# Kernel optimization log

Hardware: AMD Instinct MI355X
Metric: run time of the kernel (lower is better)

The kernel has to match this reference:

```python
import jax, jax.numpy as jnp
import numpy as np

F = 128          # num_features
NRBF = 20        # num_rbf_features
N_NODES = 25000
N_EDGES = 400000


def setup_inputs() -> dict:
    key = jax.random.key(0)
    ks = jax.random.split(key, 12)
    inp = {
        "idx_i": jax.random.randint(ks[0], (N_EDGES,), 0, N_NODES, dtype=jnp.int32),
        "idx_j": jax.random.randint(ks[1], (N_EDGES,), 0, N_NODES, dtype=jnp.int32),
        "rel_dir": jax.random.normal(ks[2], (N_EDGES, 3), dtype=jnp.float32),
        "rel_dist_cut": jax.random.uniform(ks[3], (N_EDGES,), dtype=jnp.float32),
        "rbf_features": jax.random.normal(ks[4], (N_EDGES, NRBF), dtype=jnp.float32),
        "scalar_features": jax.random.normal(ks[5], (N_NODES, F), dtype=jnp.float32),
        "vector_features": jax.random.normal(ks[6], (N_NODES, F, 3), dtype=jnp.float32),
        # scalar_network: Linear(F,F) -> SiLU -> Linear(F,3F)
        "W1": jax.random.normal(ks[7], (F, F), dtype=jnp.float32) / np.sqrt(F),
        "b1": jnp.zeros((F,), dtype=jnp.float32),
        "W2": jax.random.normal(ks[8], (3 * F, F), dtype=jnp.float32) / np.sqrt(F),
        "b2": jnp.zeros((3 * F,), dtype=jnp.float32),
        # rbf_network: Linear(NRBF, 3F)
        "Wr": jax.random.normal(ks[9], (3 * F, NRBF), dtype=jnp.float32) / np.sqrt(NRBF),
        "br": jnp.zeros((3 * F,), dtype=jnp.float32),
    }
    return inp


def reference(idx_i, idx_j, rel_dir, rel_dist_cut, rbf_features,
              scalar_features, vector_features, W1, b1, W2, b2, Wr, br):
    n_nodes = scalar_features.shape[0]
    # phi: per-node MLP -> [N, 3F]
    h = jax.nn.silu(scalar_features @ W1.T + b1)
    phi = h @ W2.T + b2
    # W: RBF-derived edge weights gated by cosine-cut distance -> [E, 3F]
    W = (rbf_features @ Wr.T + br) * rel_dist_cut[:, None]
    phi_W = phi[idx_j] * W                                  # [E, 3F]
    phi_W_vv, phi_W_ss, phi_W_vs = jnp.split(phi_W, 3, axis=-1)
    # scatter-add scalar residuals
    scalar_res = jax.ops.segment_sum(phi_W_ss, idx_i, num_segments=n_nodes)
    # per-edge vector messages [E, F, 3]
    vec_per_edge = (vector_features[idx_j] * phi_W_vv[..., None]
                    + phi_W_vs[..., None] * rel_dir[:, None, :])
    vector_res = jax.ops.segment_sum(vec_per_edge, idx_i, num_segments=n_nodes)
    return scalar_features + scalar_res, vector_features + vector_res
```

## Files before the change

### kernel.cpp

```cpp
#include <hip/hip_runtime.h>
#include <hip/hip_fp16.h>

#define F 128
#define F3 384
#define NRBF 20
#define NPB 16
#define CHUNK 64
#define PSN 32

typedef unsigned int u32;
typedef _Float16 half8 __attribute__((ext_vector_type(8)));
typedef float floatx4 __attribute__((ext_vector_type(4)));

__device__ __forceinline__ float2 uph(u32 u) {
    __half2 h = *(__half2*)&u;
    return __half22float2(h);
}
__device__ __forceinline__ u32 pkh(float a, float b) {
    __half2 h = __floats2half2_rn(a, b);
    return *(u32*)&h;
}

__device__ __forceinline__ float fdot2f(u32 a, u32 b, float c) {
#if defined(__has_builtin)
#if __has_builtin(__builtin_amdgcn_fdot2)
    typedef _Float16 h2 __attribute__((ext_vector_type(2)));
    return __builtin_amdgcn_fdot2(*(h2*)&a, *(h2*)&b, c, false);
#else
    float2 fa = uph(a), fb = uph(b);
    return fmaf(fa.x, fb.x, fmaf(fa.y, fb.y, c));
#endif
#else
    float2 fa = uph(a), fb = uph(b);
    return fmaf(fa.x, fb.x, fmaf(fa.y, fb.y, c));
#endif
}

__global__ void prep2_kernel(const float* __restrict__ Wr,
                             const float* __restrict__ W1, const float* __restrict__ W2,
                             u32* __restrict__ WrTh, _Float16* __restrict__ Wh,
                             const int* __restrict__ idx_i, int* __restrict__ counts,
                             int n_edges, int PKB) {
    int blk = blockIdx.x, tid = threadIdx.x;
    if (blk >= PKB) {
        int e = (blk - PKB) * 256 + tid;
        if (e < n_edges) atomicAdd(&counts[idx_i[e]], 1);
        return;
    }
    int t = blk * 256 + tid;
    if (t < 10 * F3) {
        int rr = t / F3, f = t % F3;
        WrTh[rr * F3 + f] = pkh(Wr[f * NRBF + 2 * rr], Wr[f * NRBF + 2 * rr + 1]);
        return;
    }
    int u = t - 10 * F3;
    if (u < (F + F3) * F) {
        int n = u >> 7, k = u & (F - 1);
        float w = (n < F) ? W1[n * F + k] : W2[(size_t)(n - F) * F + k];
        Wh[u] = (_Float16)w;
    }
}

#define SCAN_T 1024
#define SCAN_MAXN 25600
__launch_bounds__(SCAN_T)
__global__ void scan_lds_kernel(const int* __restrict__ counts, int* __restrict__ row_start,
                                int* __restrict__ cursor, int n) {
    __shared__ int sbuf[SCAN_MAXN];
    __shared__ int partial[SCAN_T];
    int t = threadIdx.x;
    for (int i = t; i < n; i += SCAN_T) sbuf[i] = counts[i];
    __syncthreads();
    int C = (n + SCAN_T - 1) / SCAN_T;
    int beg = t * C, end = min(beg + C, n);
    int sum = 0;
    for (int i = beg; i < end; i++) sum += sbuf[i];
    partial[t] = sum;
    __syncthreads();
    for (int off = 1; off < SCAN_T; off <<= 1) {
        int v = (t >= off) ? partial[t - off] : 0;
        __syncthreads();
        partial[t] += v;
        __syncthreads();
    }
    int base = (t == 0) ? 0 : partial[t - 1];
    for (int i = beg; i < end; i++) { int c = sbuf[i]; sbuf[i] = base; base += c; }
    __syncthreads();
    for (int i = t; i < n; i += SCAN_T) { int v = sbuf[i]; row_start[i] = v; cursor[i] = v; }
    if (t == SCAN_T - 1) row_start[n] = partial[SCAN_T - 1];
}

__launch_bounds__(1024)
__global__ void scan_kernel(const int* __restrict__ counts, int* __restrict__ row_start,
                            int* __restrict__ cursor, int n) {
    __shared__ int partial[1024];
    int t = threadIdx.x;
    int C = (n + 1023) / 1024;
    int beg = t * C, end = min(beg + C, n);
    int sum = 0;
    for (int i = beg; i < end; i++) sum += counts[i];
    partial[t] = sum;
    __syncthreads();
    for (int off = 1; off < 1024; off <<= 1) {
        int v = (t >= off) ? partial[t - off] : 0;
        __syncthreads();
        partial[t] += v;
        __syncthreads();
    }
    int base = (t == 0) ? 0 : partial[t - 1];
    for (int i = beg; i < end; i++) {
        int c = counts[i];
        row_start[i] = base; cursor[i] = base; base += c;
    }
    if (t == 1023) row_start[n] = partial[1023];
}

__global__ void scatter_kernel(const int* __restrict__ idx_i, int* __restrict__ cursor,
                               int* __restrict__ edge_order, int n_edges) {
    int e = blockIdx.x * blockDim.x + threadIdx.x;
    if (e < n_edges) {
        int p = atomicAdd(&cursor[idx_i[e]], 1);
        edge_order[p] = e;
    }
}

__launch_bounds__(128)
__global__ void phi_stage_kernel(const float* __restrict__ sf,
                                 const _Float16* __restrict__ Wh,
                                 const float* __restrict__ b1, const float* __restrict__ b2,
                                 const float* __restrict__ vf, __half* __restrict__ gbufh,
                                 int n_nodes) {
    __shared__ __align__(16) _Float16 stage[PSN * 768];
    _Float16 (*hl)[16][136] = reinterpret_cast<_Float16 (*)[16][136]>(stage);

    int tid = threadIdx.x;
    int lane = tid & 63;
    int wv = tid >> 6;
    int col = lane & 15;
    int kg = lane >> 4;
    int base = blockIdx.x * PSN;
    int row0 = base + wv * 16;

    half8 a1[4];
#pragma unroll
    for (int kb = 0; kb < 4; kb++) {
        int rr = row0 + col;
        if (rr >= n_nodes) rr = n_nodes - 1;
        const float4* xp = (const float4*)(sf + (size_t)rr * F + kb * 32 + kg * 8);
        float4 x0 = xp[0], x1 = xp[1];
        half8 a;
        a[0] = (_Float16)x0.x; a[1] = (_Float16)x0.y; a[2] = (_Float16)x0.z; a[3] = (_Float16)x0.w;
        a[4] = (_Float16)x1.x; a[5] = (_Float16)x1.y; a[6] = (_Float16)x1.z; a[7] = (_Float16)x1.w;
        a1[kb] = a;
    }

    floatx4 acc[8];
#pragma unroll
    for (int nt = 0; nt < 8; nt++) acc[nt] = (floatx4){0.f, 0.f, 0.f, 0.f};
#pragma unroll
    for (int nt = 0; nt < 8; nt++) {
#pragma unroll
        for (int kb = 0; kb < 4; kb++) {
            half8 b = *(const half8*)(Wh + (size_t)(nt * 16 + col) * F + kb * 32 + kg * 8);
            acc[nt] = __builtin_amdgcn_mfma_f32_16x16x32_f16(a1[kb], b, acc[nt], 0, 0, 0);
        }
    }
#pragma unroll
    for (int nt = 0; nt < 8; nt++) {
        int f1 = nt * 16 + col;
        float bb = b1[f1];
#pragma unroll
        for (int r = 0; r < 4; r++) {
            float v = acc[nt][r] + bb;
            float s = v / (1.f + __expf(-v));
            hl[wv][kg * 4 + r][f1] = (_Float16)s;
        }
    }
    __syncthreads();

    half8 a2[4];
#pragma unroll
    for (int kb = 0; kb < 4; kb++)
        a2[kb] = *(const half8*)&hl[wv][col][kb * 32 + kg * 8];
    __syncthreads();

#pragma unroll
    for (int c = 0; c < 3; c++) {
#pragma unroll
        for (int nt = 0; nt < 8; nt++) acc[nt] = (floatx4){0.f, 0.f, 0.f, 0.f};
#pragma unroll
        for (int nt = 0; nt < 8; nt++) {
#pragma unroll
            for (int kb = 0; kb < 4; kb++) {
                half8 b = *(const half8*)(Wh + (size_t)(F + c * 128 + nt * 16 + col) * F + kb * 32 + kg * 8);
                acc[nt] = __builtin_amdgcn_mfma_f32_16x16x32_f16(a2[kb], b, acc[nt], 0, 0, 0);
            }
        }
#pragma unroll
        for (int nt = 0; nt < 8; nt++) {
            int f2 = c * 128 + nt * 16 + col;
            float bb = b2[f2];
            int slot = (f2 & 63) * 12 + ((f2 >> 6) & 1) * 6 + (f2 >> 7);
#pragma unroll
            for (int r = 0; r < 4; r++) {
                int nl = wv * 16 + kg * 4 + r;
                stage[nl * 768 + slot] = (_Float16)(acc[nt][r] + bb);
            }
        }
    }

    for (int idx = tid; idx < PSN * 64; idx += 128) {
        int nl = idx >> 6, ln = idx & 63;
        int node = base + nl;
        if (node < n_nodes) {
            const float* v = vf + (size_t)node * F3;
            _Float16* s = stage + nl * 768 + ln * 12;
            s[3]  = (_Float16)v[ln * 3 + 0];
            s[4]  = (_Float16)v[ln * 3 + 1];
            s[5]  = (_Float16)v[ln * 3 + 2];
            s[9]  = (_Float16)v[(ln + 64) * 3 + 0];
            s[10] = (_Float16)v[(ln + 64) * 3 + 1];
            s[11] = (_Float16)v[(ln + 64) * 3 + 2];
        }
    }
    __syncthreads();

    const uint4* s4 = (const uint4*)stage;
    uint4* g4 = (uint4*)gbufh + (size_t)base * 96;
    for (int t = tid; t < PSN * 96; t += 128) {
        int node = base + t / 96;
        if (node < n_nodes) g4[t] = s4[t];
    }
}

__launch_bounds__(256)
__global__ void gather7_kernel(const int* __restrict__ idx_j,
                               const float* __restrict__ rel_dir, const float* __restrict__ rdc,
                               const float* __restrict__ rbf,
                               const float* __restrict__ sf, const float* __restrict__ vf,
                               const u32* __restrict__ WrTh, const float* __restrict__ br,
                               const u32* __restrict__ gbuf,
                               const int* __restrict__ row_start, const int* __restrict__ edge_order,
                               float* __restrict__ out_s, float* __restrict__ out_v,
                               int n_nodes) {
    __shared__ u32 lsm[4][CHUNK * 16];
    int tid = threadIdx.x;
    int lane = tid & 63;
    int wvid = tid >> 6;
    int w = wvid & 1;
    int node = blockIdx.x * 2 + (wvid >> 1);
    if (node >= n_nodes) return;
    u32* lds = lsm[wvid];

    int fb = lane + 64 * w;
    u32 wrpk[3][10];
    float brv[3];
#pragma unroll
    for (int k = 0; k < 3; k++) {
        brv[k] = br[fb + 128 * k];
#pragma unroll
        for (int rr = 0; rr < 10; rr++)
            wrpk[k][rr] = WrTh[rr * F3 + fb + 128 * k];
    }

    float acc_s = 0.f, av0 = 0.f, av1 = 0.f, av2 = 0.f;
    int beg = row_start[node];
    int end = row_start[node + 1];

    for (int cb = beg; cb < end; cb += CHUNK) {
        int cnt = min(CHUNK, end - cb);

        if (lane < cnt) {
            int e = edge_order[cb + lane];
            int j = idx_j[e];
            float rd = rdc[e];
            float d0 = rel_dir[e * 3 + 0], d1 = rel_dir[e * 3 + 1], d2 = rel_dir[e * 3 + 2];
            const float4* rp = (const float4*)(rbf + (size_t)e * NRBF);
            float4 r0 = rp[0], r1 = rp[1], r2 = rp[2], r3 = rp[3], r4 = rp[4];
            uint4* rec = (uint4*)(lds + lane * 16);
            rec[0] = make_uint4((u32)j, __float_as_uint(rd), __float_as_uint(d0), __float_as_uint(d1));
            rec[1] = make_uint4(__float_as_uint(d2), pkh(r0.x, r0.y), pkh(r0.z, r0.w), pkh(r1.x, r1.y));
            rec[2] = make_uint4(pkh(r1.z, r1.w), pkh(r2.x, r2.y), pkh(r2.z, r2.w), pkh(r3.x, r3.y));
            rec[3] = make_uint4(pkh(r3.z, r3.w), pkh(r4.x, r4.y), pkh(r4.z, r4.w), 0u);
        }

        auto issueL = [&](u32& g0, u32& g1, u32& g2, int m) {
            if (m < cnt) {
                int j = (int)lds[m * 16];
                const u32* gp = gbuf + (size_t)j * 384 + lane * 6 + w * 3;
                g0 = gp[0]; g1 = gp[1]; g2 = gp[2];
            }
        };
        auto computeE = [&](u32 g0, u32 g1, u32 g2, int m) {
            const uint4* q = (const uint4*)(lds + m * 16);
            uint4 q0 = q[0], q1 = q[1], q2 = q[2], q3 = q[3];
            float rd = __uint_as_float(q0.y);
            float dx = __uint_as_float(q0.z);
            float dy = __uint_as_float(q0.w);
            float dz = __uint_as_float(q1.x);
            u32 rbu[10] = { q1.y, q1.z, q1.w, q2.x, q2.y, q2.z, q2.w, q3.x, q3.y, q3.z };
            float W0 = brv[0], W1f = brv[1], W2f = brv[2];
#pragma unroll
            for (int rr = 0; rr < 10; rr++) {
                W0  = fdot2f(rbu[rr], wrpk[0][rr], W0);
                W1f = fdot2f(rbu[rr], wrpk[1][rr], W1f);
                W2f = fdot2f(rbu[rr], wrpk[2][rr], W2f);
            }
            float2 p01  = uph(g0);
            float2 p2v0 = uph(g1);
            float2 v12  = uph(g2);
            float pw0 = W0  * rd * p01.x;
            float pw1 = W1f * rd * p01.y;
            float pw2 = W2f * rd * p2v0.x;
            acc_s += pw1;
            av0 += p2v0.y * pw0 + pw2 * dx;
            av1 += v12.x  * pw0 + pw2 * dy;
            av2 += v12.y  * pw0 + pw2 * dz;
        };

        u32 A0, A1, A2, B0, B1, B2, C0, C1, C2, D0, D1, D2;
        issueL(A0, A1, A2, 0); issueL(B0, B1, B2, 1);
        issueL(C0, C1, C2, 2); issueL(D0, D1, D2, 3);
        int m = 0;
        while (true) {
            if (m >= cnt) break; computeE(A0, A1, A2, m); m++; issueL(A0, A1, A2, m + 3);
            if (m >= cnt) break; computeE(B0, B1, B2, m); m++; issueL(B0, B1, B2, m + 3);
            if (m >= cnt) break; computeE(C0, C1, C2, m); m++; issueL(C0, C1, C2, m + 3);
            if (m >= cnt) break; computeE(D0, D1, D2, m); m++; issueL(D0, D1, D2, m + 3);
        }
    }

    out_s[(size_t)node * F + fb] = sf[(size_t)node * F + fb] + acc_s;
    const float* vfi = vf + (size_t)node * F3 + fb * 3;
    float* ovi = out_v + (size_t)node * F3 + fb * 3;
    ovi[0] = vfi[0] + av0;
    ovi[1] = vfi[1] + av1;
    ovi[2] = vfi[2] + av2;
}

__global__ void transpose_wr(const float* __restrict__ Wr, float* __restrict__ WrT) {
    int idx = blockIdx.x * blockDim.x + threadIdx.x;
    if (idx < F3 * NRBF) {
        int f = idx / NRBF, r = idx % NRBF;
        WrT[r * F3 + f] = Wr[idx];
    }
}

__global__ void init_out(const float* __restrict__ sf, const float* __restrict__ vf,
                         float* __restrict__ out, int n_scalar, int n_total) {
    int i = blockIdx.x * blockDim.x + threadIdx.x;
    int n4 = n_total >> 2;
    if (i < n4) {
        float4 v;
        int base = i << 2;
        if (base < n_scalar) v = ((const float4*)sf)[i];
        else                 v = ((const float4*)vf)[i - (n_scalar >> 2)];
        ((float4*)out)[i] = v;
    }
}

__launch_bounds__(256)
__global__ void phi32_kernel(const float* __restrict__ sf,
                             const float* __restrict__ W1, const float* __restrict__ b1,
                             const float* __restrict__ W2, const float* __restrict__ b2,
                             float* __restrict__ phi, int n_nodes) {
    __shared__ float xs[NPB][F];
    __shared__ float hs[NPB][F];
    int tid = threadIdx.x;
    int nb = blockIdx.x * NPB;
    for (int t = tid; t < NPB * F / 4; t += 256) {
        int n  = t / (F / 4);
        int k4 = t % (F / 4);
        float4 v = make_float4(0.f, 0.f, 0.f, 0.f);
        if (nb + n < n_nodes) v = ((const float4*)(sf + (size_t)(nb + n) * F))[k4];
        ((float4*)&xs[n][0])[k4] = v;
    }
    __syncthreads();
    {
        int f = tid & (F - 1);
        int half_ = tid >> 7;
        float acc[8];
#pragma unroll
        for (int nn = 0; nn < 8; nn++) acc[nn] = 0.f;
        const float* w1row = W1 + (size_t)f * F;
        for (int k = 0; k < F; k++) {
            float w = w1row[k];
#pragma unroll
            for (int nn = 0; nn < 8; nn++)
                acc[nn] += xs[half_ * 8 + nn][k] * w;
        }
        float b = b1[f];
#pragma unroll
        for (int nn = 0; nn < 8; nn++) {
            float v = acc[nn] + b;
            hs[half_ * 8 + nn][f] = v / (1.f + __expf(-v));
        }
    }
    __syncthreads();
    for (int f = tid; f < F3; f += 256) {
        float acc[NPB];
#pragma unroll
        for (int n = 0; n < NPB; n++) acc[n] = 0.f;
        const float* w2row = W2 + (size_t)f * F;
        for (int k = 0; k < F; k++) {
            float w = w2row[k];
#pragma unroll
            for (int n = 0; n < NPB; n++)
                acc[n] += hs[n][k] * w;
        }
        float b = b2[f];
        for (int n = 0; n < NPB; n++)
            if (nb + n < n_nodes)
                phi[(size_t)(nb + n) * F3 + f] = acc[n] + b;
    }
}

__launch_bounds__(256)
__global__ void edge_kernel(const int* __restrict__ idx_i, const int* __restrict__ idx_j,
                            const float* __restrict__ rel_dir, const float* __restrict__ rdc,
                            const float* __restrict__ rbf,
                            const float* __restrict__ vf,
                            const float* __restrict__ WrT, const float* __restrict__ br,
                            const float* __restrict__ phi,
                            float* __restrict__ out_s, float* __restrict__ out_v,
                            int n_edges) {
    int lane = threadIdx.x & 63;
    int e = (int)((blockIdx.x * (unsigned)blockDim.x + threadIdx.x) >> 6);
    if (e >= n_edges) return;
    int i = idx_i[e], j = idx_j[e];
    float rd = rdc[e];
    float d0 = rel_dir[e * 3 + 0], d1 = rel_dir[e * 3 + 1], d2 = rel_dir[e * 3 + 2];
    float rb[NRBF];
#pragma unroll
    for (int r = 0; r < NRBF; r++) rb[r] = rbf[(size_t)e * NRBF + r];
    const float* pj = phi + (size_t)j * F3;
    float pw[6];
#pragma unroll
    for (int q = 0; q < 6; q++) {
        int f = lane + 64 * q;
        float acc = br[f];
#pragma unroll
        for (int r = 0; r < NRBF; r++)
            acc += rb[r] * WrT[r * F3 + f];
        pw[q] = acc * rd * pj[f];
    }
    atomicAdd(&out_s[(size_t)i * F + lane],       pw[2]);
    atomicAdd(&out_s[(size_t)i * F + lane + 64],  pw[3]);
    const float* vfj = vf + (size_t)j * F * 3;
    float* ovi = out_v + (size_t)i * F * 3;
#pragma unroll
    for (int h = 0; h < 2; h++) {
        int f = lane + 64 * h;
        float vv = pw[h];
        float vs = pw[4 + h];
        atomicAdd(&ovi[f * 3 + 0], vfj[f * 3 + 0] * vv + vs * d0);
        atomicAdd(&ovi[f * 3 + 1], vfj[f * 3 + 1] * vv + vs * d1);
        atomicAdd(&ovi[f * 3 + 2], vfj[f * 3 + 2] * vv + vs * d2);
    }
}

extern "C" void kernel_launch(void* const* d_in, const int* in_sizes, int n_in,
                              void* d_out, int out_size, void* d_ws, size_t ws_size,
                              hipStream_t stream) {
    const int*   idx_i   = (const int*)d_in[0];
    const int*   idx_j   = (const int*)d_in[1];
    const float* rel_dir = (const float*)d_in[2];
    const float* rdc     = (const float*)d_in[3];
    const float* rbf     = (const float*)d_in[4];
    const float* sf      = (const float*)d_in[5];
    const float* vf      = (const float*)d_in[6];
    const float* W1      = (const float*)d_in[7];
    const float* b1      = (const float*)d_in[8];
    const float* W2      = (const float*)d_in[9];
    const float* b2      = (const float*)d_in[10];
    const float* Wr      = (const float*)d_in[11];
    const float* br      = (const float*)d_in[12];

    int E = in_sizes[0];
    int N = in_sizes[5] / F;

    float* out_s = (float*)d_out;
    float* out_v = out_s + (size_t)N * F;

    size_t off = 0;
    auto slab = [&](size_t bytes) { size_t o = off; off = (off + bytes + 255) & ~(size_t)255; return o; };
    size_t o_wrth = slab((size_t)10 * F3 * sizeof(u32));
    size_t o_wh   = slab((size_t)(F + F3) * F * sizeof(_Float16));
    size_t o_gbuf = slab((size_t)N * 768 * sizeof(__half));
    size_t o_cnt  = slab((size_t)N * sizeof(int));
    size_t o_row  = slab((size_t)(N + 1) * sizeof(int));
    size_t o_ord  = slab((size_t)E * sizeof(int));
    size_t need_v7 = off;

    int pack_threads = 10 * F3 + (F + F3) * F;
    int PKB = (pack_threads + 255) / 256;
    int HB  = (E + 255) / 256;
    int PSB = (N + PSN - 1) / PSN;

    if (ws_size >= need_v7) {
        u32*      WrTh      = (u32*)((char*)d_ws + o_wrth);
        _Float16* Wh        = (_Float16*)((char*)d_ws + o_wh);
        __half*   gbufh     = (__half*)((char*)d_ws + o_gbuf);
        u32*      gbuf      = (u32*)gbufh;
        int*      counts    = (int*)((char*)d_ws + o_cnt);
        int*      cursor    = counts;
        int*      row_start = (int*)((char*)d_ws + o_row);
        int*      edge_ord  = (int*)((char*)d_ws + o_ord);

        hipMemsetAsync(counts, 0, (size_t)N * sizeof(int), stream);
        prep2_kernel<<<PKB + HB, 256, 0, stream>>>(Wr, W1, W2, WrTh, Wh, idx_i, counts, E, PKB);
        if (N <= SCAN_MAXN)
            scan_lds_kernel<<<1, SCAN_T, 0, stream>>>(counts, row_start, cursor, N);
        else
            scan_kernel<<<1, 1024, 0, stream>>>(counts, row_start, cursor, N);
        scatter_kernel<<<HB, 256, 0, stream>>>(idx_i, cursor, edge_ord, E);
        phi_stage_kernel<<<PSB, 128, 0, stream>>>(sf, Wh, b1, b2, vf, gbufh, N);
        gather7_kernel<<<(N + 1) / 2, 256, 0, stream>>>(idx_j, rel_dir, rdc, rbf, sf, vf,
                                                        WrTh, br, gbuf, row_start, edge_ord,
                                                        out_s, out_v, N);
    } else {
        size_t off2 = 0;
        auto slab2 = [&](size_t bytes) { size_t o = off2; off2 = (off2 + bytes + 255) & ~(size_t)255; return o; };
        size_t f_wrt = slab2((size_t)F3 * NRBF * sizeof(float));
        size_t f_phi = slab2((size_t)N * F3 * sizeof(float));
        float* WrT = (float*)((char*)d_ws + f_wrt);
        float* phi = (float*)((char*)d_ws + f_phi);

        int n_scalar = N * F;
        int n_total  = N * F * 4;
        init_out<<<(n_total / 4 + 255) / 256, 256, 0, stream>>>(sf, vf, (float*)d_out, n_scalar, n_total);
        transpose_wr<<<(F3 * NRBF + 255) / 256, 256, 0, stream>>>(Wr, WrT);
        phi32_kernel<<<(N + NPB - 1) / NPB, 256, 0, stream>>>(sf, W1, b1, W2, b2, phi, N);
        edge_kernel<<<(E + 3) / 4, 256, 0, stream>>>(idx_i, idx_j, rel_dir, rdc, rbf,
                                                     vf, WrT, br, phi, out_s, out_v, E);
    }
}
```

Baseline: 240.6 us.

## Prebuild sorted per-edge records in scatter and fuse with phi staging

```diff
diff --git a/kernel.cpp b/kernel.cpp
--- a/kernel.cpp
+++ b/kernel.cpp
@@ -115,30 +115,45 @@
     if (t == 1023) row_start[n] = partial[1023];
 }
 
-__global__ void scatter_kernel(const int* __restrict__ idx_i, int* __restrict__ cursor,
-                               int* __restrict__ edge_order, int n_edges) {
-    int e = blockIdx.x * blockDim.x + threadIdx.x;
-    if (e < n_edges) {
+__launch_bounds__(128)
+__global__ void stage_build_kernel(const float* __restrict__ sf,
+                                   const _Float16* __restrict__ Wh,
+                                   const float* __restrict__ b1, const float* __restrict__ b2,
+                                   const float* __restrict__ vf, __half* __restrict__ gbufh,
+                                   const int* __restrict__ idx_i, const int* __restrict__ idx_j,
+                                   const float* __restrict__ rel_dir, const float* __restrict__ rdc,
+                                   const float* __restrict__ rbf,
+                                   int* __restrict__ cursor, u32* __restrict__ recs,
+                                   int n_nodes, int n_edges, int PSB) {
+    __shared__ __align__(16) _Float16 stage[PSN * 768];
+    int blk = blockIdx.x, tid = threadIdx.x;
+
+    if (blk >= PSB) {
+        int e = (blk - PSB) * 128 + tid;
+        if (e >= n_edges) return;
         int p = atomicAdd(&cursor[idx_i[e]], 1);
-        edge_order[p] = e;
-    }
-}
-
-__launch_bounds__(128)
-__global__ void phi_stage_kernel(const float* __restrict__ sf,
-                                 const _Float16* __restrict__ Wh,
-                                 const float* __restrict__ b1, const float* __restrict__ b2,
-                                 const float* __restrict__ vf, __half* __restrict__ gbufh,
-                                 int n_nodes) {
-    __shared__ __align__(16) _Float16 stage[PSN * 768];
+        u32 r[16];
+        r[0] = (u32)idx_j[e];
+        r[1] = __float_as_uint(rdc[e]);
+        r[2] = __float_as_uint(rel_dir[e * 3 + 0]);
+        r[3] = __float_as_uint(rel_dir[e * 3 + 1]);
+        r[4] = __float_as_uint(rel_dir[e * 3 + 2]);
+        const float* rb = rbf + (size_t)e * NRBF;
+#pragma unroll
+        for (int t2 = 0; t2 < 10; t2++) r[5 + t2] = pkh(rb[2 * t2], rb[2 * t2 + 1]);
+        r[15] = 0;
+        float4* dst = (float4*)(recs + (size_t)p * 16);
+        const float4* src = (const float4*)r;
+        dst[0] = src[0]; dst[1] = src[1]; dst[2] = src[2]; dst[3] = src[3];
+        return;
+    }
+
     _Float16 (*hl)[16][136] = reinterpret_cast<_Float16 (*)[16][136]>(stage);
-
-    int tid = threadIdx.x;
     int lane = tid & 63;
     int wv = tid >> 6;
     int col = lane & 15;
     int kg = lane >> 4;
-    int base = blockIdx.x * PSN;
+    int base = blk * PSN;
     int row0 = base + wv * 16;
 
     half8 a1[4];
@@ -234,13 +249,10 @@
 }
 
 __launch_bounds__(256)
-__global__ void gather7_kernel(const int* __restrict__ idx_j,
-                               const float* __restrict__ rel_dir, const float* __restrict__ rdc,
-                               const float* __restrict__ rbf,
-                               const float* __restrict__ sf, const float* __restrict__ vf,
+__global__ void gather5_kernel(const float* __restrict__ sf, const float* __restrict__ vf,
                                const u32* __restrict__ WrTh, const float* __restrict__ br,
-                               const u32* __restrict__ gbuf,
-                               const int* __restrict__ row_start, const int* __restrict__ edge_order,
+                               const u32* __restrict__ gbuf, const u32* __restrict__ recs,
+                               const int* __restrict__ row_start,
                                float* __restrict__ out_s, float* __restrict__ out_v,
                                int n_nodes) {
     __shared__ u32 lsm[4][CHUNK * 16];
@@ -269,19 +281,11 @@
 
     for (int cb = beg; cb < end; cb += CHUNK) {
         int cnt = min(CHUNK, end - cb);
-
-        if (lane < cnt) {
-            int e = edge_order[cb + lane];
-            int j = idx_j[e];
-            float rd = rdc[e];
-            float d0 = rel_dir[e * 3 + 0], d1 = rel_dir[e * 3 + 1], d2 = rel_dir[e * 3 + 2];
-            const float4* rp = (const float4*)(rbf + (size_t)e * NRBF);
-            float4 r0 = rp[0], r1 = rp[1], r2 = rp[2], r3 = rp[3], r4 = rp[4];
-            uint4* rec = (uint4*)(lds + lane * 16);
-            rec[0] = make_uint4((u32)j, __float_as_uint(rd), __float_as_uint(d0), __float_as_uint(d1));
-            rec[1] = make_uint4(__float_as_uint(d2), pkh(r0.x, r0.y), pkh(r0.z, r0.w), pkh(r1.x, r1.y));
-            rec[2] = make_uint4(pkh(r1.z, r1.w), pkh(r2.x, r2.y), pkh(r2.z, r2.w), pkh(r3.x, r3.y));
-            rec[3] = make_uint4(pkh(r3.z, r3.w), pkh(r4.x, r4.y), pkh(r4.z, r4.w), 0u);
+        {
+            const float4* src = (const float4*)(recs + (size_t)cb * 16);
+            int nf4 = cnt * 4;
+            for (int t = lane; t < nf4; t += 64)
+                ((float4*)lds)[t] = src[t];
         }
 
         auto issueL = [&](u32& g0, u32& g1, u32& g2, int m) {
@@ -489,15 +493,16 @@
     size_t o_gbuf = slab((size_t)N * 768 * sizeof(__half));
     size_t o_cnt  = slab((size_t)N * sizeof(int));
     size_t o_row  = slab((size_t)(N + 1) * sizeof(int));
-    size_t o_ord  = slab((size_t)E * sizeof(int));
-    size_t need_v7 = off;
+    size_t o_rec  = slab((size_t)E * 64);
+    size_t need_v8 = off;
 
     int pack_threads = 10 * F3 + (F + F3) * F;
     int PKB = (pack_threads + 255) / 256;
     int HB  = (E + 255) / 256;
     int PSB = (N + PSN - 1) / PSN;
-
-    if (ws_size >= need_v7) {
+    int BB  = (E + 127) / 128;
+
+    if (ws_size >= need_v8) {
         u32*      WrTh      = (u32*)((char*)d_ws + o_wrth);
         _Float16* Wh        = (_Float16*)((char*)d_ws + o_wh);
         __half*   gbufh     = (__half*)((char*)d_ws + o_gbuf);
@@ -505,7 +510,7 @@
         int*      counts    = (int*)((char*)d_ws + o_cnt);
         int*      cursor    = counts;
         int*      row_start = (int*)((char*)d_ws + o_row);
-        int*      edge_ord  = (int*)((char*)d_ws + o_ord);
+        u32*      recs      = (u32*)((char*)d_ws + o_rec);
 
         hipMemsetAsync(counts, 0, (size_t)N * sizeof(int), stream);
         prep2_kernel<<<PKB + HB, 256, 0, stream>>>(Wr, W1, W2, WrTh, Wh, idx_i, counts, E, PKB);
@@ -513,11 +518,11 @@
             scan_lds_kernel<<<1, SCAN_T, 0, stream>>>(counts, row_start, cursor, N);
         else
             scan_kernel<<<1, 1024, 0, stream>>>(counts, row_start, cursor, N);
-        scatter_kernel<<<HB, 256, 0, stream>>>(idx_i, cursor, edge_ord, E);
-        phi_stage_kernel<<<PSB, 128, 0, stream>>>(sf, Wh, b1, b2, vf, gbufh, N);
-        gather7_kernel<<<(N + 1) / 2, 256, 0, stream>>>(idx_j, rel_dir, rdc, rbf, sf, vf,
-                                                        WrTh, br, gbuf, row_start, edge_ord,
-                                                        out_s, out_v, N);
+        stage_build_kernel<<<PSB + BB, 128, 0, stream>>>(sf, Wh, b1, b2, vf, gbufh,
+                                                         idx_i, idx_j, rel_dir, rdc, rbf,
+                                                         cursor, recs, N, E, PSB);
+        gather5_kernel<<<(N + 1) / 2, 256, 0, stream>>>(sf, vf, WrTh, br, gbuf, recs,
+                                                        row_start, out_s, out_v, N);
     } else {
         size_t off2 = 0;
         auto slab2 = [&](size_t bytes) { size_t o = off2; off2 = (off2 + bytes + 255) & ~(size_t)255; return o; };
```

New measurement: 205.8 us. 1.17x faster.
